# Kernel optimization log

Measured on AMD Instinct MI355X. Metric: run time of the kernel, lower is better.

## Reference

```python
import jax, jax.numpy as jnp
import numpy as np

N_NODES = 100000


def setup_inputs() -> dict:
    key = jax.random.key(0)
    k1, k2, k3, k4 = jax.random.split(key, 4)
    E = 3200000
    D = 16
    x = jax.random.uniform(k1, (N_NODES, D), dtype=jnp.float32)
    edge_index = jax.random.randint(k2, (2, E), 0, N_NODES, dtype=jnp.int64)
    edge_probs = jax.random.uniform(k3, (E,), dtype=jnp.float32)
    weight = jnp.ones((D,), dtype=jnp.float32)
    self_loop_weight = jnp.asarray(0.1, dtype=jnp.float32)
    return {"x": x, "edge_index": edge_index, "edge_probs": edge_probs,
            "weight": weight, "self_loop_weight": self_loop_weight}


def reference(x, edge_index, edge_probs, weight, self_loop_weight):
    src = edge_index[0]
    dst = edge_index[1]
    # gather + elementwise: [E, D]
    messages = x[src] * edge_probs[:, None] * weight
    # scatter_add over destination nodes -> [N, D]
    out = jax.ops.segment_sum(messages, dst, num_segments=N_NODES)
    out = out + x * self_loop_weight
    return jnp.clip(x + out, 0.0, 1.0)
```

## Files before the change

kernel.cpp:

```cpp
#include <hip/hip_runtime.h>
#include <hip/hip_fp16.h>

#define N_NODES 100000
#define DIM 16
#define BSHIFT 7
#define BNODES 128
#define NB ((N_NODES + BNODES - 1) / BNODES)
#define TB 512
#define CHUNK 8192
#define CAPB 4608
#define QSCALE 32767.0f


__global__ __launch_bounds__(256) void convert_x_kernel(const float* __restrict__ x,
                                                        __half* __restrict__ xh,
                                                        int n8) {
    int i = blockIdx.x * 256 + threadIdx.x;
    if (i >= n8) return;
    float4 a = ((const float4*)x)[2 * i];
    float4 b = ((const float4*)x)[2 * i + 1];
    __half2 h0 = __floats2half2_rn(a.x, a.y);
    __half2 h1 = __floats2half2_rn(a.z, a.w);
    __half2 h2 = __floats2half2_rn(b.x, b.y);
    __half2 h3 = __floats2half2_rn(b.z, b.w);
    uint4 u;
    u.x = *reinterpret_cast<unsigned*>(&h0);
    u.y = *reinterpret_cast<unsigned*>(&h1);
    u.z = *reinterpret_cast<unsigned*>(&h2);
    u.w = *reinterpret_cast<unsigned*>(&h3);
    ((uint4*)xh)[i] = u;
}

__global__ __launch_bounds__(TB) void hist_kernel(const int* __restrict__ dst,
                                                  unsigned* __restrict__ H,
                                                  int E) {
    __shared__ unsigned hist[NB];
    int tid = threadIdx.x;
    for (int i = tid; i < NB; i += TB) hist[i] = 0;
    __syncthreads();
    int e0 = blockIdx.x * CHUNK;
    int e1 = min(e0 + CHUNK, E);
    for (int e = e0 + tid; e < e1; e += TB)
        atomicAdd(&hist[((unsigned)dst[e]) >> BSHIFT], 1u);
    __syncthreads();
    unsigned* row = H + (size_t)blockIdx.x * NB;
    for (int i = tid; i < NB; i += TB) row[i] = hist[i];
}

__device__ inline unsigned block_scan_excl(unsigned v, int tid, int nthreads,
                                           unsigned* warp_lds, unsigned* total_out) {
    unsigned x = v;
#pragma unroll
    for (int off = 1; off < 64; off <<= 1) {
        unsigned y = __shfl_up(x, off);
        if ((tid & 63) >= off) x += y;
    }
    int wid = tid >> 6;
    int nw = nthreads >> 6;
    if ((tid & 63) == 63) warp_lds[wid] = x;
    __syncthreads();
    if (tid < nw) {
        unsigned w = warp_lds[tid];
#pragma unroll
        for (int off = 1; off < 16; off <<= 1) {
            unsigned y = __shfl_up(w, off);
            if (tid >= off) w += y;
        }
        warp_lds[tid] = w;
    }
    __syncthreads();
    unsigned wbase = (wid > 0) ? warp_lds[wid - 1] : 0u;
    unsigned incl = x + wbase;
    if (total_out && tid == nthreads - 1) *total_out = incl;
    return incl - v;
}

__global__ __launch_bounds__(TB) void scan_wg_kernel(unsigned* __restrict__ H,
                                                     unsigned* __restrict__ totals,
                                                     int nwg) {
    __shared__ unsigned warp_lds[16];
    int b = blockIdx.x;
    int tid = threadIdx.x;
    unsigned v = (tid < nwg) ? H[(size_t)tid * NB + b] : 0u;
    unsigned excl = block_scan_excl(v, tid, TB, warp_lds, &totals[b]);
    if (tid < nwg) H[(size_t)tid * NB + b] = excl;
}

__global__ __launch_bounds__(1024) void scan_bucket_kernel(const unsigned* __restrict__ totals,
                                                           unsigned* __restrict__ base) {
    __shared__ unsigned warp_lds[16];
    int tid = threadIdx.x;
    unsigned v = (tid < NB) ? totals[tid] : 0u;
    unsigned excl = block_scan_excl(v, tid, 1024, warp_lds, nullptr);
    if (tid < NB) base[tid] = excl;
}

__global__ __launch_bounds__(TB) void place_kernel(const int* __restrict__ src,
                                                   const int* __restrict__ dst,
                                                   const float* __restrict__ probs,
                                                   const unsigned* __restrict__ O,
                                                   const unsigned* __restrict__ totals,
                                                   const unsigned* __restrict__ base,
                                                   unsigned char* __restrict__ key,
                                                   unsigned* __restrict__ payload,
                                                   int E, int nwg) {
    __shared__ unsigned recs_pl[CHUNK];
    __shared__ unsigned char recs_k[CHUNK];
    __shared__ unsigned lstart[NB];
    __shared__ unsigned lcur[NB];
    __shared__ unsigned gdst[NB];
    __shared__ unsigned warp_lds[16];
    int tid = threadIdx.x;
    int wg = blockIdx.x;
    int e0 = wg * CHUNK;
    int e1 = min(e0 + CHUNK, E);
    bool last = (wg == nwg - 1);

    const unsigned* row  = O + (size_t)wg * NB;
    const unsigned* rown = O + (size_t)(wg + 1) * NB;
    for (int i = tid; i < NB; i += TB) {
        unsigned h = row[i];
        unsigned hn = last ? totals[i] : rown[i];
        gdst[i] = base[i] + h;
        lcur[i] = hn - h;
    }
    __syncthreads();

    int b0 = 2 * tid, b1 = 2 * tid + 1;
    unsigned c0 = (b0 < NB) ? lcur[b0] : 0u;
    unsigned c1 = (b1 < NB) ? lcur[b1] : 0u;
    unsigned excl = block_scan_excl(c0 + c1, tid, TB, warp_lds, nullptr);
    __syncthreads();
    if (b0 < NB) { lstart[b0] = excl;      lcur[b0] = excl; }
    if (b1 < NB) { lstart[b1] = excl + c0; lcur[b1] = excl + c0; }
    __syncthreads();

    for (int e = e0 + tid; e < e1; e += TB) {
        unsigned d = (unsigned)dst[e];
        unsigned s = (unsigned)src[e];
        float p = probs[e];
        unsigned b = d >> BSHIFT;
        unsigned pos = atomicAdd(&lcur[b], 1u);
        unsigned q = __float2uint_rn(p * QSCALE);
        recs_pl[pos] = (s << 15) | q;
        recs_k[pos] = (unsigned char)(d & (BNODES - 1));
    }
    __syncthreads();

    int wv = tid >> 6, ln = tid & 63;
    int bq = ln >> 4, ln16 = ln & 15;
    for (int bb = wv * 4; bb < NB; bb += (TB >> 6) * 4) {
        int b = bb + bq;
        unsigned st = 0, cnt = 0, g = 0;
        if (b < NB) { st = lstart[b]; cnt = lcur[b] - st; g = gdst[b]; }
        for (unsigned k = ln16; k < cnt; k += 16) {
            payload[g + k] = recs_pl[st + k];
            key[g + k]     = recs_k[st + k];
        }
    }
}

__global__ __launch_bounds__(TB) void sort_gather_kernel(const float* __restrict__ x,
                                                         const __half* __restrict__ xh,
                                                         const float* __restrict__ weight,
                                                         const float* __restrict__ slw,
                                                         const unsigned* __restrict__ base,
                                                         const unsigned* __restrict__ totals,
                                                         const unsigned char* __restrict__ key,
                                                         const unsigned* __restrict__ payload,
                                                         float* __restrict__ out) {
    __shared__ unsigned buf[CAPB];
    __shared__ float accs[BNODES * DIM];
    __shared__ unsigned ncnt[BNODES];
    __shared__ unsigned nstart[BNODES];
    __shared__ unsigned ncur[BNODES];
    int tid = threadIdx.x;
    int b = blockIdx.x;
    unsigned s0 = base[b];
    unsigned cnt = totals[b];
    int wv = tid >> 6, lane = tid & 63;
    int sub = lane >> 3, dc = lane & 7;
    const __half2* xh2 = (const __half2*)xh;
    const float QS = 1.0f / QSCALE;

    for (int i = tid; i < BNODES * DIM; i += TB) accs[i] = 0.0f;

    for (unsigned t0 = 0; t0 < cnt; t0 += CAPB) {
        unsigned tcnt = min((unsigned)CAPB, cnt - t0);
        unsigned g0 = s0 + t0;
        if (tid < BNODES) ncnt[tid] = 0;
        __syncthreads();
        for (unsigned i = tid; i < tcnt; i += TB)
            atomicAdd(&ncnt[key[g0 + i]], 1u);
        __syncthreads();
        if (tid < 64) {
            unsigned c0 = ncnt[2 * tid], c1 = ncnt[2 * tid + 1];
            unsigned v = c0 + c1;
            unsigned xs = v;
#pragma unroll
            for (int off = 1; off < 64; off <<= 1) {
                unsigned y = __shfl_up(xs, off);
                if (tid >= off) xs += y;
            }
            nstart[2 * tid]     = xs - v;  ncur[2 * tid]     = xs - v;
            nstart[2 * tid + 1] = xs - c1; ncur[2 * tid + 1] = xs - c1;
        }
        __syncthreads();
        for (unsigned i = tid; i < tcnt; i += TB) {
            unsigned k = key[g0 + i];
            unsigned pos = atomicAdd(&ncur[k], 1u);
            buf[pos] = payload[g0 + i];
        }
        __syncthreads();
        for (int nloc = wv; nloc < BNODES; nloc += (TB >> 6)) {
            unsigned lo = nstart[nloc];
            unsigned hi = lo + ncnt[nloc];
            float ax = 0.0f, ay = 0.0f;
            for (unsigned i = lo + (unsigned)sub; i < hi; i += 32) {
                unsigned r0 = buf[i];
                unsigned r1 = (i + 8  < hi) ? buf[i + 8]  : 0u;
                unsigned r2 = (i + 16 < hi) ? buf[i + 16] : 0u;
                unsigned r3 = (i + 24 < hi) ? buf[i + 24] : 0u;
                float2 f0 = __half22float2(xh2[(size_t)(r0 >> 15) * 8 + dc]);
                float2 f1 = __half22float2(xh2[(size_t)(r1 >> 15) * 8 + dc]);
                float2 f2 = __half22float2(xh2[(size_t)(r2 >> 15) * 8 + dc]);
                float2 f3 = __half22float2(xh2[(size_t)(r3 >> 15) * 8 + dc]);
                float p0 = (float)(r0 & 0x7FFFu) * QS;
                float p1 = (float)(r1 & 0x7FFFu) * QS;
                float p2 = (float)(r2 & 0x7FFFu) * QS;
                float p3 = (float)(r3 & 0x7FFFu) * QS;
                ax = fmaf(f0.x, p0, ax); ay = fmaf(f0.y, p0, ay);
                ax = fmaf(f1.x, p1, ax); ay = fmaf(f1.y, p1, ay);
                ax = fmaf(f2.x, p2, ax); ay = fmaf(f2.y, p2, ay);
                ax = fmaf(f3.x, p3, ax); ay = fmaf(f3.y, p3, ay);
            }
            ax += __shfl_xor(ax, 8);  ay += __shfl_xor(ay, 8);
            ax += __shfl_xor(ax, 16); ay += __shfl_xor(ay, 16);
            ax += __shfl_xor(ax, 32); ay += __shfl_xor(ay, 32);
            if (lane < 8) {
                float2* a2 = (float2*)&accs[nloc * DIM + 2 * dc];
                float2 cur = *a2;
                cur.x += ax; cur.y += ay;
                *a2 = cur;
            }
        }
        __syncthreads();
    }

    float sc = 1.0f + slw[0];
    for (int idx = tid; idx < BNODES * 8; idx += TB) {
        int nloc = idx >> 3, q = idx & 7;
        int n = b * BNODES + nloc;
        if (n >= N_NODES) continue;
        float2 a = ((float2*)accs)[nloc * 8 + q];
        float2 xv = ((const float2*)x)[(size_t)n * 8 + q];
        float2 wv2 = ((const float2*)weight)[q];
        float2 r;
        r.x = fminf(fmaxf(fmaf(xv.x, sc, a.x * wv2.x), 0.0f), 1.0f);
        r.y = fminf(fmaxf(fmaf(xv.y, sc, a.y * wv2.y), 0.0f), 1.0f);
        ((float2*)out)[(size_t)n * 8 + q] = r;
    }
}


__global__ void diffusion_scatter_kernel(const float* __restrict__ x,
                                         const int* __restrict__ src,
                                         const int* __restrict__ dst,
                                         const float* __restrict__ probs,
                                         const float* __restrict__ weight,
                                         float* __restrict__ acc,
                                         int E) {
    int e = blockIdx.x * blockDim.x + threadIdx.x;
    if (e >= E) return;
    int s = src[e];
    int d = dst[e];
    float p = probs[e];
    const float4* xs = reinterpret_cast<const float4*>(x + (size_t)s * DIM);
    const float4* w4 = reinterpret_cast<const float4*>(weight);
    float* outp = acc + (size_t)d * DIM;
#pragma unroll
    for (int q = 0; q < 4; ++q) {
        float4 xv = xs[q];
        float4 wv = w4[q];
        atomicAdd(&outp[q * 4 + 0], xv.x * p * wv.x);
        atomicAdd(&outp[q * 4 + 1], xv.y * p * wv.y);
        atomicAdd(&outp[q * 4 + 2], xv.z * p * wv.z);
        atomicAdd(&outp[q * 4 + 3], xv.w * p * wv.w);
    }
}

__global__ void diffusion_finalize_kernel(const float* __restrict__ x,
                                          const float* __restrict__ slw,
                                          float* __restrict__ out,
                                          int n4) {
    int i = blockIdx.x * blockDim.x + threadIdx.x;
    if (i >= n4) return;
    float s = 1.0f + slw[0];
    float4 xv = reinterpret_cast<const float4*>(x)[i];
    float4 a = reinterpret_cast<float4*>(out)[i];
    float4 r;
    r.x = fminf(fmaxf(fmaf(xv.x, s, a.x), 0.0f), 1.0f);
    r.y = fminf(fmaxf(fmaf(xv.y, s, a.y), 0.0f), 1.0f);
    r.z = fminf(fmaxf(fmaf(xv.z, s, a.z), 0.0f), 1.0f);
    r.w = fminf(fmaxf(fmaf(xv.w, s, a.w), 0.0f), 1.0f);
    reinterpret_cast<float4*>(out)[i] = r;
}

extern "C" void kernel_launch(void* const* d_in, const int* in_sizes, int n_in,
                              void* d_out, int out_size, void* d_ws, size_t ws_size,
                              hipStream_t stream) {
    const float* x      = (const float*)d_in[0];
    const int*   eidx   = (const int*)d_in[1];
    const float* probs  = (const float*)d_in[2];
    const float* weight = (const float*)d_in[3];
    const float* slw    = (const float*)d_in[4];

    int E = in_sizes[2];
    float* out = (float*)d_out;

    int nwg = (E + CHUNK - 1) / CHUNK;

    size_t off = 0;
    auto alloc = [&](size_t bytes) { size_t o = off; off += (bytes + 15) & ~(size_t)15; return o; };
    size_t o_H       = alloc((size_t)nwg * NB * 4);
    size_t o_totals  = alloc((size_t)NB * 4);
    size_t o_base    = alloc((size_t)NB * 4);
    size_t o_xh      = alloc((size_t)N_NODES * DIM * 2);
    size_t o_key     = alloc((size_t)E);
    size_t o_payload = alloc((size_t)E * 4);
    size_t need = off;

    if (ws_size >= need && nwg <= TB) {
        char* ws = (char*)d_ws;
        unsigned* H           = (unsigned*)(ws + o_H);
        unsigned* totals      = (unsigned*)(ws + o_totals);
        unsigned* basep       = (unsigned*)(ws + o_base);
        __half*   xh          = (__half*)(ws + o_xh);
        unsigned char* key    = (unsigned char*)(ws + o_key);
        unsigned* payload     = (unsigned*)(ws + o_payload);

        int n8 = N_NODES * DIM / 8;
        convert_x_kernel<<<(n8 + 255) / 256, 256, 0, stream>>>(x, xh, n8);
        hist_kernel<<<nwg, TB, 0, stream>>>(eidx + E, H, E);
        scan_wg_kernel<<<NB, TB, 0, stream>>>(H, totals, nwg);
        scan_bucket_kernel<<<1, 1024, 0, stream>>>(totals, basep);
        place_kernel<<<nwg, TB, 0, stream>>>(eidx, eidx + E, probs, H, totals, basep,
                                             key, payload, E, nwg);
        sort_gather_kernel<<<NB, TB, 0, stream>>>(x, xh, weight, slw, basep, totals,
                                                  key, payload, out);
    } else {
        const int T = 256;
        hipMemsetAsync(d_out, 0, (size_t)out_size * sizeof(float), stream);
        diffusion_scatter_kernel<<<(E + T - 1) / T, T, 0, stream>>>(
            x, eidx, eidx + E, probs, weight, out, E);
        int n4 = out_size / 4;
        diffusion_finalize_kernel<<<(n4 + T - 1) / T, T, 0, stream>>>(
            x, slw, out, n4);
    }
}
```

Baseline: 83.82 us.

## Replace per-bucket local sort with split LDS-atomic accumulation plus finalize pass

Drops the in-block counting sort of each 128-node bucket. Each bucket's edge range is now split across four 256-thread blocks that accumulate directly into padded shared memory with float atomics. A separate finalize kernel sums the four partials and applies the self-loop, weight and clamp. The aim is more parallelism (four times as many blocks) and removal of the histogram, scan and scatter passes with their barriers, at the cost of LDS atomic contention, an extra partial buffer round trip through global memory, and one more kernel launch.

```diff
diff --git a/kernel.cpp b/kernel.cpp
--- a/kernel.cpp
+++ b/kernel.cpp
@@ -8,8 +8,9 @@
 #define NB ((N_NODES + BNODES - 1) / BNODES)
 #define TB 512
 #define CHUNK 8192
-#define CAPB 4608
 #define QSCALE 32767.0f
+#define SPLIT 4
+#define ASTRIDE 17
 
 
 __global__ __launch_bounds__(256) void convert_x_kernel(const float* __restrict__ x,
@@ -160,106 +161,89 @@
     }
 }
 
-__global__ __launch_bounds__(TB) void sort_gather_kernel(const float* __restrict__ x,
-                                                         const __half* __restrict__ xh,
-                                                         const float* __restrict__ weight,
-                                                         const float* __restrict__ slw,
-                                                         const unsigned* __restrict__ base,
-                                                         const unsigned* __restrict__ totals,
-                                                         const unsigned char* __restrict__ key,
-                                                         const unsigned* __restrict__ payload,
-                                                         float* __restrict__ out) {
-    __shared__ unsigned buf[CAPB];
-    __shared__ float accs[BNODES * DIM];
-    __shared__ unsigned ncnt[BNODES];
-    __shared__ unsigned nstart[BNODES];
-    __shared__ unsigned ncur[BNODES];
-    int tid = threadIdx.x;
-    int b = blockIdx.x;
+__global__ __launch_bounds__(256) void accum_kernel(const __half* __restrict__ xh,
+                                                    const unsigned* __restrict__ base,
+                                                    const unsigned* __restrict__ totals,
+                                                    const unsigned char* __restrict__ key,
+                                                    const unsigned* __restrict__ payload,
+                                                    float* __restrict__ partial) {
+    __shared__ float accs[BNODES * ASTRIDE];
+    int tid = threadIdx.x;
+    int bs = blockIdx.x;
+    int b = bs >> 2;
+    int sub = bs & 3;
+    for (int i = tid; i < BNODES * ASTRIDE; i += 256) accs[i] = 0.0f;
+    __syncthreads();
+
     unsigned s0 = base[b];
     unsigned cnt = totals[b];
-    int wv = tid >> 6, lane = tid & 63;
-    int sub = lane >> 3, dc = lane & 7;
+    unsigned lo = s0 + (cnt * (unsigned)sub) / SPLIT;
+    unsigned hi = s0 + (cnt * (unsigned)(sub + 1)) / SPLIT;
+
+    int grp = tid >> 3;
+    int dc  = tid & 7;
     const __half2* xh2 = (const __half2*)xh;
     const float QS = 1.0f / QSCALE;
 
-    for (int i = tid; i < BNODES * DIM; i += TB) accs[i] = 0.0f;
-
-    for (unsigned t0 = 0; t0 < cnt; t0 += CAPB) {
-        unsigned tcnt = min((unsigned)CAPB, cnt - t0);
-        unsigned g0 = s0 + t0;
-        if (tid < BNODES) ncnt[tid] = 0;
-        __syncthreads();
-        for (unsigned i = tid; i < tcnt; i += TB)
-            atomicAdd(&ncnt[key[g0 + i]], 1u);
-        __syncthreads();
-        if (tid < 64) {
-            unsigned c0 = ncnt[2 * tid], c1 = ncnt[2 * tid + 1];
-            unsigned v = c0 + c1;
-            unsigned xs = v;
+    for (unsigned i = lo + (unsigned)grp; i < hi; i += 128) {
+        unsigned i1 = i + 32, i2 = i + 64, i3 = i + 96;
+        unsigned r0 = payload[i];
+        unsigned k0 = key[i];
+        unsigned r1 = (i1 < hi) ? payload[i1] : 0u;
+        unsigned k1 = (i1 < hi) ? key[i1] : 0u;
+        unsigned r2 = (i2 < hi) ? payload[i2] : 0u;
+        unsigned k2 = (i2 < hi) ? key[i2] : 0u;
+        unsigned r3 = (i3 < hi) ? payload[i3] : 0u;
+        unsigned k3 = (i3 < hi) ? key[i3] : 0u;
+        float2 f0 = __half22float2(xh2[(size_t)(r0 >> 15) * 8 + dc]);
+        float2 f1 = __half22float2(xh2[(size_t)(r1 >> 15) * 8 + dc]);
+        float2 f2 = __half22float2(xh2[(size_t)(r2 >> 15) * 8 + dc]);
+        float2 f3 = __half22float2(xh2[(size_t)(r3 >> 15) * 8 + dc]);
+        float p0 = (float)(r0 & 0x7FFFu) * QS;
+        float p1 = (float)(r1 & 0x7FFFu) * QS;
+        float p2 = (float)(r2 & 0x7FFFu) * QS;
+        float p3 = (float)(r3 & 0x7FFFu) * QS;
+        atomicAdd(&accs[k0 * ASTRIDE + 2 * dc],     f0.x * p0);
+        atomicAdd(&accs[k0 * ASTRIDE + 2 * dc + 1], f0.y * p0);
+        atomicAdd(&accs[k1 * ASTRIDE + 2 * dc],     f1.x * p1);
+        atomicAdd(&accs[k1 * ASTRIDE + 2 * dc + 1], f1.y * p1);
+        atomicAdd(&accs[k2 * ASTRIDE + 2 * dc],     f2.x * p2);
+        atomicAdd(&accs[k2 * ASTRIDE + 2 * dc + 1], f2.y * p2);
+        atomicAdd(&accs[k3 * ASTRIDE + 2 * dc],     f3.x * p3);
+        atomicAdd(&accs[k3 * ASTRIDE + 2 * dc + 1], f3.y * p3);
+    }
+    __syncthreads();
+    float* prow = partial + (size_t)bs * (BNODES * DIM);
+    for (int k = tid; k < BNODES * DIM; k += 256)
+        prow[k] = accs[(k >> 4) * ASTRIDE + (k & 15)];
+}
+
+__global__ __launch_bounds__(256) void finalize_kernel(const float* __restrict__ x,
+                                                       const float* __restrict__ weight,
+                                                       const float* __restrict__ slw,
+                                                       const float* __restrict__ partial,
+                                                       float* __restrict__ out) {
+    int i = blockIdx.x * 256 + threadIdx.x;
+    int n = i >> 2, q = i & 3;
+    if (n >= N_NODES) return;
+    int b = n >> BSHIFT;
+    int nloc = n & (BNODES - 1);
+    float4 wv = ((const float4*)weight)[q];
+    float4 a = make_float4(0.f, 0.f, 0.f, 0.f);
+    size_t pbase = (size_t)(b * SPLIT) * (BNODES * DIM) + (size_t)nloc * DIM + q * 4;
 #pragma unroll
-            for (int off = 1; off < 64; off <<= 1) {
-                unsigned y = __shfl_up(xs, off);
-                if (tid >= off) xs += y;
-            }
-            nstart[2 * tid]     = xs - v;  ncur[2 * tid]     = xs - v;
-            nstart[2 * tid + 1] = xs - c1; ncur[2 * tid + 1] = xs - c1;
-        }
-        __syncthreads();
-        for (unsigned i = tid; i < tcnt; i += TB) {
-            unsigned k = key[g0 + i];
-            unsigned pos = atomicAdd(&ncur[k], 1u);
-            buf[pos] = payload[g0 + i];
-        }
-        __syncthreads();
-        for (int nloc = wv; nloc < BNODES; nloc += (TB >> 6)) {
-            unsigned lo = nstart[nloc];
-            unsigned hi = lo + ncnt[nloc];
-            float ax = 0.0f, ay = 0.0f;
-            for (unsigned i = lo + (unsigned)sub; i < hi; i += 32) {
-                unsigned r0 = buf[i];
-                unsigned r1 = (i + 8  < hi) ? buf[i + 8]  : 0u;
-                unsigned r2 = (i + 16 < hi) ? buf[i + 16] : 0u;
-                unsigned r3 = (i + 24 < hi) ? buf[i + 24] : 0u;
-                float2 f0 = __half22float2(xh2[(size_t)(r0 >> 15) * 8 + dc]);
-                float2 f1 = __half22float2(xh2[(size_t)(r1 >> 15) * 8 + dc]);
-                float2 f2 = __half22float2(xh2[(size_t)(r2 >> 15) * 8 + dc]);
-                float2 f3 = __half22float2(xh2[(size_t)(r3 >> 15) * 8 + dc]);
-                float p0 = (float)(r0 & 0x7FFFu) * QS;
-                float p1 = (float)(r1 & 0x7FFFu) * QS;
-                float p2 = (float)(r2 & 0x7FFFu) * QS;
-                float p3 = (float)(r3 & 0x7FFFu) * QS;
-                ax = fmaf(f0.x, p0, ax); ay = fmaf(f0.y, p0, ay);
-                ax = fmaf(f1.x, p1, ax); ay = fmaf(f1.y, p1, ay);
-                ax = fmaf(f2.x, p2, ax); ay = fmaf(f2.y, p2, ay);
-                ax = fmaf(f3.x, p3, ax); ay = fmaf(f3.y, p3, ay);
-            }
-            ax += __shfl_xor(ax, 8);  ay += __shfl_xor(ay, 8);
-            ax += __shfl_xor(ax, 16); ay += __shfl_xor(ay, 16);
-            ax += __shfl_xor(ax, 32); ay += __shfl_xor(ay, 32);
-            if (lane < 8) {
-                float2* a2 = (float2*)&accs[nloc * DIM + 2 * dc];
-                float2 cur = *a2;
-                cur.x += ax; cur.y += ay;
-                *a2 = cur;
-            }
-        }
-        __syncthreads();
-    }
-
+    for (int s = 0; s < SPLIT; ++s) {
+        float4 pv = *(const float4*)(partial + pbase + (size_t)s * (BNODES * DIM));
+        a.x += pv.x; a.y += pv.y; a.z += pv.z; a.w += pv.w;
+    }
     float sc = 1.0f + slw[0];
-    for (int idx = tid; idx < BNODES * 8; idx += TB) {
-        int nloc = idx >> 3, q = idx & 7;
-        int n = b * BNODES + nloc;
-        if (n >= N_NODES) continue;
-        float2 a = ((float2*)accs)[nloc * 8 + q];
-        float2 xv = ((const float2*)x)[(size_t)n * 8 + q];
-        float2 wv2 = ((const float2*)weight)[q];
-        float2 r;
-        r.x = fminf(fmaxf(fmaf(xv.x, sc, a.x * wv2.x), 0.0f), 1.0f);
-        r.y = fminf(fmaxf(fmaf(xv.y, sc, a.y * wv2.y), 0.0f), 1.0f);
-        ((float2*)out)[(size_t)n * 8 + q] = r;
-    }
+    float4 xv = ((const float4*)x)[i];
+    float4 r;
+    r.x = fminf(fmaxf(fmaf(xv.x, sc, a.x * wv.x), 0.0f), 1.0f);
+    r.y = fminf(fmaxf(fmaf(xv.y, sc, a.y * wv.y), 0.0f), 1.0f);
+    r.z = fminf(fmaxf(fmaf(xv.z, sc, a.z * wv.z), 0.0f), 1.0f);
+    r.w = fminf(fmaxf(fmaf(xv.w, sc, a.w * wv.w), 0.0f), 1.0f);
+    ((float4*)out)[i] = r;
 }
 
 
@@ -328,6 +312,7 @@
     size_t o_xh      = alloc((size_t)N_NODES * DIM * 2);
     size_t o_key     = alloc((size_t)E);
     size_t o_payload = alloc((size_t)E * 4);
+    size_t o_partial = alloc((size_t)NB * SPLIT * BNODES * DIM * 4);
     size_t need = off;
 
     if (ws_size >= need && nwg <= TB) {
@@ -338,6 +323,7 @@
         __half*   xh          = (__half*)(ws + o_xh);
         unsigned char* key    = (unsigned char*)(ws + o_key);
         unsigned* payload     = (unsigned*)(ws + o_payload);
+        float*    partial     = (float*)(ws + o_partial);
 
         int n8 = N_NODES * DIM / 8;
         convert_x_kernel<<<(n8 + 255) / 256, 256, 0, stream>>>(x, xh, n8);
@@ -346,8 +332,11 @@
         scan_bucket_kernel<<<1, 1024, 0, stream>>>(totals, basep);
         place_kernel<<<nwg, TB, 0, stream>>>(eidx, eidx + E, probs, H, totals, basep,
                                              key, payload, E, nwg);
-        sort_gather_kernel<<<NB, TB, 0, stream>>>(x, xh, weight, slw, basep, totals,
-                                                  key, payload, out);
+        accum_kernel<<<NB * SPLIT, 256, 0, stream>>>(xh, basep, totals, key, payload,
+                                                     partial);
+        int nquad = N_NODES * 4;
+        finalize_kernel<<<(nquad + 255) / 256, 256, 0, stream>>>(
+            x, weight, slw, partial, out);
     } else {
         const int T = 256;
         hipMemsetAsync(d_out, 0, (size_t)out_size * sizeof(float), stream);
```

Result: slower. 334.3 us (+298.8%).

## Fuse x fp16 conversion into histogram kernel and interleave two nodes per wave

Applied to the files above, without the earlier changes.

Folds the x-to-fp16 conversion into the histogram kernel as a grid-stride loop, removing one kernel launch. In the gather phase each wave now processes two destination nodes (nloc and nloc+8) concurrently, issuing twice as many independent gather loads per iteration to hide memory latency. This raises register pressure, and the interleaved loop runs until the longer of the two segments ends, which wastes lanes when the two node counts differ.

```diff
diff --git a/kernel.cpp b/kernel.cpp
--- a/kernel.cpp
+++ b/kernel.cpp
@@ -12,28 +12,29 @@
 #define QSCALE 32767.0f
 
 
-__global__ __launch_bounds__(256) void convert_x_kernel(const float* __restrict__ x,
-                                                        __half* __restrict__ xh,
-                                                        int n8) {
-    int i = blockIdx.x * 256 + threadIdx.x;
-    if (i >= n8) return;
-    float4 a = ((const float4*)x)[2 * i];
-    float4 b = ((const float4*)x)[2 * i + 1];
-    __half2 h0 = __floats2half2_rn(a.x, a.y);
-    __half2 h1 = __floats2half2_rn(a.z, a.w);
-    __half2 h2 = __floats2half2_rn(b.x, b.y);
-    __half2 h3 = __floats2half2_rn(b.z, b.w);
-    uint4 u;
-    u.x = *reinterpret_cast<unsigned*>(&h0);
-    u.y = *reinterpret_cast<unsigned*>(&h1);
-    u.z = *reinterpret_cast<unsigned*>(&h2);
-    u.w = *reinterpret_cast<unsigned*>(&h3);
-    ((uint4*)xh)[i] = u;
-}
-
-__global__ __launch_bounds__(TB) void hist_kernel(const int* __restrict__ dst,
+__global__ __launch_bounds__(TB) void hist_kernel(const float* __restrict__ x,
+                                                  __half* __restrict__ xh,
+                                                  int n8,
+                                                  const int* __restrict__ dst,
                                                   unsigned* __restrict__ H,
                                                   int E) {
+    int gid = blockIdx.x * TB + threadIdx.x;
+    int gsz = gridDim.x * TB;
+    for (int i = gid; i < n8; i += gsz) {
+        float4 a = ((const float4*)x)[2 * i];
+        float4 b = ((const float4*)x)[2 * i + 1];
+        __half2 h0 = __floats2half2_rn(a.x, a.y);
+        __half2 h1 = __floats2half2_rn(a.z, a.w);
+        __half2 h2 = __floats2half2_rn(b.x, b.y);
+        __half2 h3 = __floats2half2_rn(b.z, b.w);
+        uint4 u;
+        u.x = *reinterpret_cast<unsigned*>(&h0);
+        u.y = *reinterpret_cast<unsigned*>(&h1);
+        u.z = *reinterpret_cast<unsigned*>(&h2);
+        u.w = *reinterpret_cast<unsigned*>(&h3);
+        ((uint4*)xh)[i] = u;
+    }
+
     __shared__ unsigned hist[NB];
     int tid = threadIdx.x;
     for (int i = tid; i < NB; i += TB) hist[i] = 0;
@@ -212,36 +213,61 @@
             buf[pos] = payload[g0 + i];
         }
         __syncthreads();
-        for (int nloc = wv; nloc < BNODES; nloc += (TB >> 6)) {
-            unsigned lo = nstart[nloc];
-            unsigned hi = lo + ncnt[nloc];
-            float ax = 0.0f, ay = 0.0f;
-            for (unsigned i = lo + (unsigned)sub; i < hi; i += 32) {
-                unsigned r0 = buf[i];
-                unsigned r1 = (i + 8  < hi) ? buf[i + 8]  : 0u;
-                unsigned r2 = (i + 16 < hi) ? buf[i + 16] : 0u;
-                unsigned r3 = (i + 24 < hi) ? buf[i + 24] : 0u;
-                float2 f0 = __half22float2(xh2[(size_t)(r0 >> 15) * 8 + dc]);
-                float2 f1 = __half22float2(xh2[(size_t)(r1 >> 15) * 8 + dc]);
-                float2 f2 = __half22float2(xh2[(size_t)(r2 >> 15) * 8 + dc]);
-                float2 f3 = __half22float2(xh2[(size_t)(r3 >> 15) * 8 + dc]);
-                float p0 = (float)(r0 & 0x7FFFu) * QS;
-                float p1 = (float)(r1 & 0x7FFFu) * QS;
-                float p2 = (float)(r2 & 0x7FFFu) * QS;
-                float p3 = (float)(r3 & 0x7FFFu) * QS;
-                ax = fmaf(f0.x, p0, ax); ay = fmaf(f0.y, p0, ay);
-                ax = fmaf(f1.x, p1, ax); ay = fmaf(f1.y, p1, ay);
-                ax = fmaf(f2.x, p2, ax); ay = fmaf(f2.y, p2, ay);
-                ax = fmaf(f3.x, p3, ax); ay = fmaf(f3.y, p3, ay);
+        for (int nloc = wv; nloc < BNODES; nloc += 16) {
+            int nlocB = nloc + 8;
+            unsigned loA = nstart[nloc];
+            unsigned hiA = loA + ncnt[nloc];
+            unsigned loB = nstart[nlocB];
+            unsigned hiB = loB + ncnt[nlocB];
+            float axA = 0.0f, ayA = 0.0f, axB = 0.0f, ayB = 0.0f;
+            unsigned iA = loA + (unsigned)sub;
+            unsigned iB = loB + (unsigned)sub;
+            while (iA < hiA || iB < hiB) {
+                unsigned a0 = (iA      < hiA) ? buf[iA]      : 0u;
+                unsigned a1 = (iA + 8  < hiA) ? buf[iA + 8]  : 0u;
+                unsigned a2 = (iA + 16 < hiA) ? buf[iA + 16] : 0u;
+                unsigned a3 = (iA + 24 < hiA) ? buf[iA + 24] : 0u;
+                unsigned b0 = (iB      < hiB) ? buf[iB]      : 0u;
+                unsigned b1 = (iB + 8  < hiB) ? buf[iB + 8]  : 0u;
+                unsigned b2 = (iB + 16 < hiB) ? buf[iB + 16] : 0u;
+                unsigned b3 = (iB + 24 < hiB) ? buf[iB + 24] : 0u;
+                float2 fa0 = __half22float2(xh2[(size_t)(a0 >> 15) * 8 + dc]);
+                float2 fa1 = __half22float2(xh2[(size_t)(a1 >> 15) * 8 + dc]);
+                float2 fa2 = __half22float2(xh2[(size_t)(a2 >> 15) * 8 + dc]);
+                float2 fa3 = __half22float2(xh2[(size_t)(a3 >> 15) * 8 + dc]);
+                float2 fb0 = __half22float2(xh2[(size_t)(b0 >> 15) * 8 + dc]);
+                float2 fb1 = __half22float2(xh2[(size_t)(b1 >> 15) * 8 + dc]);
+                float2 fb2 = __half22float2(xh2[(size_t)(b2 >> 15) * 8 + dc]);
+                float2 fb3 = __half22float2(xh2[(size_t)(b3 >> 15) * 8 + dc]);
+                float pa0 = (float)(a0 & 0x7FFFu) * QS;
+                float pa1 = (float)(a1 & 0x7FFFu) * QS;
+                float pa2 = (float)(a2 & 0x7FFFu) * QS;
+                float pa3 = (float)(a3 & 0x7FFFu) * QS;
+                float pb0 = (float)(b0 & 0x7FFFu) * QS;
+                float pb1 = (float)(b1 & 0x7FFFu) * QS;
+                float pb2 = (float)(b2 & 0x7FFFu) * QS;
+                float pb3 = (float)(b3 & 0x7FFFu) * QS;
+                axA = fmaf(fa0.x, pa0, axA); ayA = fmaf(fa0.y, pa0, ayA);
+                axA = fmaf(fa1.x, pa1, axA); ayA = fmaf(fa1.y, pa1, ayA);
+                axA = fmaf(fa2.x, pa2, axA); ayA = fmaf(fa2.y, pa2, ayA);
+                axA = fmaf(fa3.x, pa3, axA); ayA = fmaf(fa3.y, pa3, ayA);
+                axB = fmaf(fb0.x, pb0, axB); ayB = fmaf(fb0.y, pb0, ayB);
+                axB = fmaf(fb1.x, pb1, axB); ayB = fmaf(fb1.y, pb1, ayB);
+                axB = fmaf(fb2.x, pb2, axB); ayB = fmaf(fb2.y, pb2, ayB);
+                axB = fmaf(fb3.x, pb3, axB); ayB = fmaf(fb3.y, pb3, ayB);
+                iA += 32; iB += 32;
             }
-            ax += __shfl_xor(ax, 8);  ay += __shfl_xor(ay, 8);
-            ax += __shfl_xor(ax, 16); ay += __shfl_xor(ay, 16);
-            ax += __shfl_xor(ax, 32); ay += __shfl_xor(ay, 32);
+            axA += __shfl_xor(axA, 8);  ayA += __shfl_xor(ayA, 8);
+            axB += __shfl_xor(axB, 8);  ayB += __shfl_xor(ayB, 8);
+            axA += __shfl_xor(axA, 16); ayA += __shfl_xor(ayA, 16);
+            axB += __shfl_xor(axB, 16); ayB += __shfl_xor(ayB, 16);
+            axA += __shfl_xor(axA, 32); ayA += __shfl_xor(ayA, 32);
+            axB += __shfl_xor(axB, 32); ayB += __shfl_xor(ayB, 32);
             if (lane < 8) {
-                float2* a2 = (float2*)&accs[nloc * DIM + 2 * dc];
-                float2 cur = *a2;
-                cur.x += ax; cur.y += ay;
-                *a2 = cur;
+                float2* aA = (float2*)&accs[nloc * DIM + 2 * dc];
+                float2 cA = *aA; cA.x += axA; cA.y += ayA; *aA = cA;
+                float2* aB = (float2*)&accs[nlocB * DIM + 2 * dc];
+                float2 cB = *aB; cB.x += axB; cB.y += ayB; *aB = cB;
             }
         }
         __syncthreads();
@@ -340,8 +366,7 @@
         unsigned* payload     = (unsigned*)(ws + o_payload);
 
         int n8 = N_NODES * DIM / 8;
-        convert_x_kernel<<<(n8 + 255) / 256, 256, 0, stream>>>(x, xh, n8);
-        hist_kernel<<<nwg, TB, 0, stream>>>(eidx + E, H, E);
+        hist_kernel<<<nwg, TB, 0, stream>>>(x, xh, n8, eidx + E, H, E);
         scan_wg_kernel<<<NB, TB, 0, stream>>>(H, totals, nwg);
         scan_bucket_kernel<<<1, 1024, 0, stream>>>(totals, basep);
         place_kernel<<<nwg, TB, 0, stream>>>(eidx, eidx + E, probs, H, totals, basep,
```

New measurement: 80.00 us. 4.6% less time.

## Fuse x conversion into histogram, merge bucket scan via last-block, vectorize edge loads

Applied to the files above, without the earlier changes.

Folds the fp32-to-fp16 conversion of x into the histogram kernel and replaces the separate bucket-scan launch with a last-block-done pattern in the per-bucket scan kernel, cutting two kernel launches. The histogram and placement loops now read dst, src and probs as int4/float4 quads. The sort-gather kernel caches keys in LDS so they are read from global memory only once. The atomic counter with threadfence adds some serialization risk, and the extra kbuf array raises LDS use per block.

```diff
diff --git a/kernel.cpp b/kernel.cpp
--- a/kernel.cpp
+++ b/kernel.cpp
@@ -12,35 +12,47 @@
 #define QSCALE 32767.0f
 
 
-__global__ __launch_bounds__(256) void convert_x_kernel(const float* __restrict__ x,
-                                                        __half* __restrict__ xh,
-                                                        int n8) {
-    int i = blockIdx.x * 256 + threadIdx.x;
-    if (i >= n8) return;
-    float4 a = ((const float4*)x)[2 * i];
-    float4 b = ((const float4*)x)[2 * i + 1];
-    __half2 h0 = __floats2half2_rn(a.x, a.y);
-    __half2 h1 = __floats2half2_rn(a.z, a.w);
-    __half2 h2 = __floats2half2_rn(b.x, b.y);
-    __half2 h3 = __floats2half2_rn(b.z, b.w);
-    uint4 u;
-    u.x = *reinterpret_cast<unsigned*>(&h0);
-    u.y = *reinterpret_cast<unsigned*>(&h1);
-    u.z = *reinterpret_cast<unsigned*>(&h2);
-    u.w = *reinterpret_cast<unsigned*>(&h3);
-    ((uint4*)xh)[i] = u;
-}
-
-__global__ __launch_bounds__(TB) void hist_kernel(const int* __restrict__ dst,
+__global__ __launch_bounds__(TB) void hist_kernel(const float* __restrict__ x,
+                                                  __half* __restrict__ xh,
+                                                  int n8,
+                                                  const int* __restrict__ dst,
                                                   unsigned* __restrict__ H,
+                                                  unsigned* __restrict__ done,
                                                   int E) {
+    if (blockIdx.x == 0 && threadIdx.x == 0) *done = 0u;
+
+    int gid = blockIdx.x * TB + threadIdx.x;
+    int gsz = gridDim.x * TB;
+    for (int i = gid; i < n8; i += gsz) {
+        float4 a = ((const float4*)x)[2 * i];
+        float4 b = ((const float4*)x)[2 * i + 1];
+        __half2 h0 = __floats2half2_rn(a.x, a.y);
+        __half2 h1 = __floats2half2_rn(a.z, a.w);
+        __half2 h2 = __floats2half2_rn(b.x, b.y);
+        __half2 h3 = __floats2half2_rn(b.z, b.w);
+        uint4 u;
+        u.x = *reinterpret_cast<unsigned*>(&h0);
+        u.y = *reinterpret_cast<unsigned*>(&h1);
+        u.z = *reinterpret_cast<unsigned*>(&h2);
+        u.w = *reinterpret_cast<unsigned*>(&h3);
+        ((uint4*)xh)[i] = u;
+    }
+
     __shared__ unsigned hist[NB];
     int tid = threadIdx.x;
     for (int i = tid; i < NB; i += TB) hist[i] = 0;
     __syncthreads();
     int e0 = blockIdx.x * CHUNK;
     int e1 = min(e0 + CHUNK, E);
-    for (int e = e0 + tid; e < e1; e += TB)
+    int nquad = ((E & 3) == 0) ? ((e1 - e0) >> 2) : 0;
+    for (int qi = tid; qi < nquad; qi += TB) {
+        int4 d4 = *(const int4*)(dst + e0 + qi * 4);
+        atomicAdd(&hist[((unsigned)d4.x) >> BSHIFT], 1u);
+        atomicAdd(&hist[((unsigned)d4.y) >> BSHIFT], 1u);
+        atomicAdd(&hist[((unsigned)d4.z) >> BSHIFT], 1u);
+        atomicAdd(&hist[((unsigned)d4.w) >> BSHIFT], 1u);
+    }
+    for (int e = e0 + nquad * 4 + tid; e < e1; e += TB)
         atomicAdd(&hist[((unsigned)dst[e]) >> BSHIFT], 1u);
     __syncthreads();
     unsigned* row = H + (size_t)blockIdx.x * NB;
@@ -77,22 +89,30 @@
 
 __global__ __launch_bounds__(TB) void scan_wg_kernel(unsigned* __restrict__ H,
                                                      unsigned* __restrict__ totals,
+                                                     unsigned* __restrict__ base,
+                                                     unsigned* __restrict__ done,
                                                      int nwg) {
     __shared__ unsigned warp_lds[16];
+    __shared__ unsigned is_last;
     int b = blockIdx.x;
     int tid = threadIdx.x;
     unsigned v = (tid < nwg) ? H[(size_t)tid * NB + b] : 0u;
-    unsigned excl = block_scan_excl(v, tid, TB, warp_lds, &totals[b]);
+    unsigned excl = block_scan_excl(v, tid, TB, warp_lds, nullptr);
     if (tid < nwg) H[(size_t)tid * NB + b] = excl;
-}
-
-__global__ __launch_bounds__(1024) void scan_bucket_kernel(const unsigned* __restrict__ totals,
-                                                           unsigned* __restrict__ base) {
-    __shared__ unsigned warp_lds[16];
-    int tid = threadIdx.x;
-    unsigned v = (tid < NB) ? totals[tid] : 0u;
-    unsigned excl = block_scan_excl(v, tid, 1024, warp_lds, nullptr);
-    if (tid < NB) base[tid] = excl;
+    if (tid == TB - 1) {
+        atomicExch(&totals[b], excl + v);
+        __threadfence();
+        is_last = (atomicAdd(done, 1u) == (unsigned)(NB - 1)) ? 1u : 0u;
+    }
+    __syncthreads();
+    if (is_last) {
+        int b0 = 2 * tid, b1 = 2 * tid + 1;
+        unsigned c0 = (b0 < NB) ? atomicAdd(&totals[b0], 0u) : 0u;
+        unsigned c1 = (b1 < NB) ? atomicAdd(&totals[b1], 0u) : 0u;
+        unsigned excl2 = block_scan_excl(c0 + c1, tid, TB, warp_lds, nullptr);
+        if (b0 < NB) base[b0] = excl2;
+        if (b1 < NB) base[b1] = excl2 + c0;
+    }
 }
 
 __global__ __launch_bounds__(TB) void place_kernel(const int* __restrict__ src,
@@ -135,12 +155,30 @@
     if (b1 < NB) { lstart[b1] = excl + c0; lcur[b1] = excl + c0; }
     __syncthreads();
 
-    for (int e = e0 + tid; e < e1; e += TB) {
+    int nquad = ((E & 3) == 0) ? ((e1 - e0) >> 2) : 0;
+    for (int qi = tid; qi < nquad; qi += TB) {
+        int e = e0 + qi * 4;
+        int4   s4 = *(const int4*)(src + e);
+        int4   d4 = *(const int4*)(dst + e);
+        float4 p4 = *(const float4*)(probs + e);
+#pragma unroll
+        for (int u = 0; u < 4; ++u) {
+            unsigned d = (unsigned)((&d4.x)[u]);
+            unsigned s = (unsigned)((&s4.x)[u]);
+            float p = (&p4.x)[u];
+            unsigned bb = d >> BSHIFT;
+            unsigned pos = atomicAdd(&lcur[bb], 1u);
+            unsigned q = __float2uint_rn(p * QSCALE);
+            recs_pl[pos] = (s << 15) | q;
+            recs_k[pos] = (unsigned char)(d & (BNODES - 1));
+        }
+    }
+    for (int e = e0 + nquad * 4 + tid; e < e1; e += TB) {
         unsigned d = (unsigned)dst[e];
         unsigned s = (unsigned)src[e];
         float p = probs[e];
-        unsigned b = d >> BSHIFT;
-        unsigned pos = atomicAdd(&lcur[b], 1u);
+        unsigned bb = d >> BSHIFT;
+        unsigned pos = atomicAdd(&lcur[bb], 1u);
         unsigned q = __float2uint_rn(p * QSCALE);
         recs_pl[pos] = (s << 15) | q;
         recs_k[pos] = (unsigned char)(d & (BNODES - 1));
@@ -170,6 +208,7 @@
                                                          const unsigned* __restrict__ payload,
                                                          float* __restrict__ out) {
     __shared__ unsigned buf[CAPB];
+    __shared__ unsigned char kbuf[CAPB];
     __shared__ float accs[BNODES * DIM];
     __shared__ unsigned ncnt[BNODES];
     __shared__ unsigned nstart[BNODES];
@@ -190,8 +229,11 @@
         unsigned g0 = s0 + t0;
         if (tid < BNODES) ncnt[tid] = 0;
         __syncthreads();
-        for (unsigned i = tid; i < tcnt; i += TB)
-            atomicAdd(&ncnt[key[g0 + i]], 1u);
+        for (unsigned i = tid; i < tcnt; i += TB) {
+            unsigned char k = key[g0 + i];
+            kbuf[i] = k;
+            atomicAdd(&ncnt[k], 1u);
+        }
         __syncthreads();
         if (tid < 64) {
             unsigned c0 = ncnt[2 * tid], c1 = ncnt[2 * tid + 1];
@@ -207,7 +249,7 @@
         }
         __syncthreads();
         for (unsigned i = tid; i < tcnt; i += TB) {
-            unsigned k = key[g0 + i];
+            unsigned k = kbuf[i];
             unsigned pos = atomicAdd(&ncur[k], 1u);
             buf[pos] = payload[g0 + i];
         }
@@ -325,6 +367,7 @@
     size_t o_H       = alloc((size_t)nwg * NB * 4);
     size_t o_totals  = alloc((size_t)NB * 4);
     size_t o_base    = alloc((size_t)NB * 4);
+    size_t o_done    = alloc(4);
     size_t o_xh      = alloc((size_t)N_NODES * DIM * 2);
     size_t o_key     = alloc((size_t)E);
     size_t o_payload = alloc((size_t)E * 4);
@@ -335,15 +378,14 @@
         unsigned* H           = (unsigned*)(ws + o_H);
         unsigned* totals      = (unsigned*)(ws + o_totals);
         unsigned* basep       = (unsigned*)(ws + o_base);
+        unsigned* done        = (unsigned*)(ws + o_done);
         __half*   xh          = (__half*)(ws + o_xh);
         unsigned char* key    = (unsigned char*)(ws + o_key);
         unsigned* payload     = (unsigned*)(ws + o_payload);
 
         int n8 = N_NODES * DIM / 8;
-        convert_x_kernel<<<(n8 + 255) / 256, 256, 0, stream>>>(x, xh, n8);
-        hist_kernel<<<nwg, TB, 0, stream>>>(eidx + E, H, E);
-        scan_wg_kernel<<<NB, TB, 0, stream>>>(H, totals, nwg);
-        scan_bucket_kernel<<<1, 1024, 0, stream>>>(totals, basep);
+        hist_kernel<<<nwg, TB, 0, stream>>>(x, xh, n8, eidx + E, H, done, E);
+        scan_wg_kernel<<<NB, TB, 0, stream>>>(H, totals, basep, done, nwg);
         place_kernel<<<nwg, TB, 0, stream>>>(eidx, eidx + E, probs, H, totals, basep,
                                              key, payload, E, nwg);
         sort_gather_kernel<<<NB, TB, 0, stream>>>(x, xh, weight, slw, basep, totals,
```

New measurement: 104.6 us. +24.8%, slower.
